# Kernel optimization log

Hardware: AMD Instinct MI355X
Metric: run time of the kernel (lower is better)

Reference implementation:

```python
import jax, jax.numpy as jnp
import numpy as np

SEQ, BATCH, IN_F, STATE, OUT_F = 2048, 32, 256, 512, 256


def setup_inputs() -> dict:
    key = jax.random.key(0)
    k1, k2, k3, k4 = jax.random.split(key, 4)
    x = jax.random.normal(k1, (SEQ, BATCH, IN_F), dtype=jnp.float32)
    # lambda_log init per module __init__ with rmin=0, rmax=1:
    # u ~ U(0,1); lambda_log = log(-0.5*log(u*(rmax+rmin)*(rmax-rmin)+rmin^2)) = log(-0.5*log(u))
    u = jax.random.uniform(k2, (STATE,), dtype=jnp.float32, minval=1e-6, maxval=1.0)
    lambda_log = jnp.log(-0.5 * jnp.log(u))
    B = jax.random.normal(k3, (STATE, IN_F), dtype=jnp.float32) / np.float32(np.sqrt(IN_F))
    C = jax.random.normal(k4, (OUT_F, STATE), dtype=jnp.float32) / np.float32(np.sqrt(STATE))
    return {"input": x, "lambda_log": lambda_log, "B": B, "C": C}


def reference(input, lambda_log, B, C):
    # mode='sequential', inner_loops=1, rnn_burnin=0, done=None, hidden=None
    lamda = jnp.exp(-jnp.exp(lambda_log))                 # [N]
    gamma = jnp.sqrt(1.0 - lamda * lamda + 1e-7)          # [N]
    # project all timesteps at once: b_seq[s,b,n] = gamma_n * (x_s @ B^T)
    b_seq = jnp.einsum('sbi,ni->sbn', input, B) * gamma   # [S,B,N]

    def step(state, b_t):
        new_state = lamda * state + b_t                   # diagonal LRU recurrence
        return new_state, new_state

    init = jnp.zeros((input.shape[1], lambda_log.shape[0]), dtype=input.dtype)
    final_state, states = jax.lax.scan(step, init, b_seq)  # states: [S,B,N]
    output = jnp.einsum('sbn,on->sbo', states, C)          # [S,B,O]
    return output, final_state
```

## Files before the change

kernel.cpp:

```cpp
#include <hip/hip_runtime.h>

#define SEQ   2048
#define BATCH 32
#define INF   256
#define NST   512
#define OUTF  256
#define CLEN  32
#define NCH   64
#define NJOB  4
#define NCG   (NCH / NJOB)
#define NBLK  (NCG * BATCH)

typedef __bf16 bf16;
typedef __bf16 bf16x8 __attribute__((ext_vector_type(8)));
typedef float  f32x4  __attribute__((ext_vector_type(4)));
typedef unsigned long long ull;

__global__ void k_prep(const float* __restrict__ ll,
                       const float* __restrict__ Bm,
                       const float* __restrict__ Cm,
                       float* __restrict__ lam,
                       float* __restrict__ lamG,
                       float* __restrict__ l2la,
                       bf16* __restrict__ Bb,
                       bf16* __restrict__ Cb) {
  int i = blockIdx.x * 256 + threadIdx.x;
  if (i < NST) {
    float e = expf(ll[i]);
    float lmb = expf(-e);
    lam[i] = lmb;
    l2la[i] = -e * 1.44269504088896341f;
    float p = lmb;
#pragma unroll
    for (int q = 0; q < 7; ++q) p *= p;
    lamG[i] = p;
  }
  if (i < NST * INF) {
    int n = i >> 8;
    float lmb = expf(-expf(ll[n]));
    float g = sqrtf(1.0f - lmb * lmb + 1e-7f);
    Bb[i] = (bf16)(Bm[i] * g);
  }
  if (i < OUTF * NST) {
    Cb[i] = (bf16)(Cm[i]);
  }
}

__device__ __forceinline__ void xload(const float* __restrict__ xp, int tid,
                                      float4 xr[4]) {
#pragma unroll
  for (int rep = 0; rep < 4; ++rep) {
    int slot = rep * 512 + tid;
    int row = slot >> 6, col4 = slot & 63;
    xr[rep] = *(const float4*)(xp + (size_t)row * (BATCH * INF) + col4 * 4);
  }
}

__device__ __forceinline__ void xstore(char* xsb, int tid, const float4 xr[4]) {
#pragma unroll
  for (int rep = 0; rep < 4; ++rep) {
    int slot = rep * 512 + tid;
    int row = slot >> 6, col4 = slot & 63;
    union { bf16 h[4]; ull u; } pk;
    pk.h[0] = (bf16)xr[rep].x; pk.h[1] = (bf16)xr[rep].y;
    pk.h[2] = (bf16)xr[rep].z; pk.h[3] = (bf16)xr[rep].w;
    int byte = (row * (INF * 2) + col4 * 8) ^ ((row & 15) << 4);
    *(ull*)(xsb + byte) = pk.u;
  }
}

__device__ __forceinline__ void reg_scan(f32x4 acc[2][4], float carry[4],
                                         const float la[4], const float l4[4],
                                         int kg, int rl) {
#pragma unroll
  for (int mt = 0; mt < 2; ++mt) {
    float sl[4][4];
#pragma unroll
    for (int nt = 0; nt < 4; ++nt) {
      sl[nt][0] = acc[mt][nt][0];
      sl[nt][1] = fmaf(la[nt], sl[nt][0], acc[mt][nt][1]);
      sl[nt][2] = fmaf(la[nt], sl[nt][1], acc[mt][nt][2]);
      sl[nt][3] = fmaf(la[nt], sl[nt][2], acc[mt][nt][3]);
    }
    float G[4];
#pragma unroll
    for (int nt = 0; nt < 4; ++nt) {
      float g1 = __shfl_up(sl[nt][3], 16);
      G[nt] = (kg >= 1) ? fmaf(l4[nt], g1, sl[nt][3]) : sl[nt][3];
    }
#pragma unroll
    for (int nt = 0; nt < 4; ++nt) {
      float l8 = l4[nt] * l4[nt];
      float g2 = __shfl_up(G[nt], 32);
      G[nt] = (kg >= 2) ? fmaf(l8, g2, G[nt]) : G[nt];
    }
#pragma unroll
    for (int nt = 0; nt < 4; ++nt) {
      float X = __shfl_up(G[nt], 16);
      X = (kg >= 1) ? X : 0.0f;
      float l8 = l4[nt] * l4[nt];
      float p4k = ((kg & 1) ? l4[nt] : 1.0f) * ((kg & 2) ? l8 : 1.0f);
      float cin = fmaf(p4k, carry[nt], X);
      float l2 = la[nt] * la[nt], l3 = l2 * la[nt];
      acc[mt][nt][0] = fmaf(la[nt], cin, sl[nt][0]);
      acc[mt][nt][1] = fmaf(l2, cin, sl[nt][1]);
      acc[mt][nt][2] = fmaf(l3, cin, sl[nt][2]);
      acc[mt][nt][3] = fmaf(l4[nt], cin, sl[nt][3]);
    }
#pragma unroll
    for (int nt = 0; nt < 4; ++nt)
      carry[nt] = __shfl(acc[mt][nt][3], rl + 48);
  }
}

__device__ __forceinline__ void gemm1_l2(const char* xsb, const bf16* __restrict__ Bb,
                                         f32x4 acc[2][4], int n0, int rl, int kg) {
#pragma unroll
  for (int k = 0; k < 8; ++k) {
    bf16x8 af[2], bfr[4];
#pragma unroll
    for (int mt = 0; mt < 2; ++mt) {
      int row = mt * 16 + rl;
      int byte = (row * (INF * 2) + (k * 32 + kg * 8) * 2) ^ (rl << 4);
      af[mt] = *(const bf16x8*)(xsb + byte);
    }
#pragma unroll
    for (int nt = 0; nt < 4; ++nt)
      bfr[nt] = *(const bf16x8*)(Bb + (size_t)(n0 + nt * 16 + rl) * INF + k * 32 + kg * 8);
#pragma unroll
    for (int mt = 0; mt < 2; ++mt)
#pragma unroll
      for (int nt = 0; nt < 4; ++nt)
        acc[mt][nt] = __builtin_amdgcn_mfma_f32_16x16x32_bf16(af[mt], bfr[nt], acc[mt][nt], 0, 0, 0);
  }
}

__global__ __launch_bounds__(512, 2)
void k_pass0f(const float* __restrict__ x, const bf16* __restrict__ Bb,
              const float* __restrict__ lam, float* __restrict__ Z,
              ull* __restrict__ bfrag) {
  __shared__ __align__(16) char xs[2][CLEN * INF * 2];

  const int tid = threadIdx.x, wid = tid >> 6, lane = tid & 63;
  const int rl = lane & 15, kg = lane >> 4;
  const int b = blockIdx.x >> 4, cg = blockIdx.x & 15;
  const int n0 = wid * 64;

  float la[4], l4[4], carry[4];
#pragma unroll
  for (int nt = 0; nt < 4; ++nt) {
    float v = lam[n0 + nt * 16 + rl];
    la[nt] = v; l4[nt] = (v * v) * (v * v);
    carry[nt] = 0.0f;
  }

  bf16x8 Breg[8][4];
#pragma unroll
  for (int k = 0; k < 8; ++k)
#pragma unroll
    for (int nt = 0; nt < 4; ++nt)
      Breg[k][nt] = *(const bf16x8*)(Bb + (size_t)(n0 + nt * 16 + rl) * INF + k * 32 + kg * 8);

  {
    float4 xr0[4];
    xload(x + ((size_t)(cg * NJOB * CLEN) * BATCH + b) * INF, tid, xr0);
    xstore(xs[0], tid, xr0);
  }
  __syncthreads();

#pragma unroll
  for (int jj = 0; jj < NJOB; ++jj) {
    const int c = cg * NJOB + jj;
    f32x4 acc[2][4] = {};
#pragma unroll
    for (int k = 0; k < 8; ++k) {
      bf16x8 af[2];
#pragma unroll
      for (int mt = 0; mt < 2; ++mt) {
        int row = mt * 16 + rl;
        int byte = (row * (INF * 2) + (k * 32 + kg * 8) * 2) ^ (rl << 4);
        af[mt] = *(const bf16x8*)(&xs[jj & 1][0] + byte);
      }
#pragma unroll
      for (int mt = 0; mt < 2; ++mt)
#pragma unroll
        for (int nt = 0; nt < 4; ++nt)
          acc[mt][nt] = __builtin_amdgcn_mfma_f32_16x16x32_bf16(af[mt], Breg[k][nt], acc[mt][nt], 0, 0, 0);
    }

    float4 xr[4];
    if (jj < NJOB - 1)
      xload(x + ((size_t)((c + 1) * CLEN) * BATCH + b) * INF, tid, xr);

    reg_scan(acc, carry, la, l4, kg, rl);

    {
      ull* dst = bfrag + ((size_t)(((cg * BATCH + b) * NJOB + jj) * 8 + wid)) * 512 + lane;
#pragma unroll
      for (int mt = 0; mt < 2; ++mt)
#pragma unroll
        for (int nt = 0; nt < 4; ++nt) {
          union { bf16 h[4]; ull u; } pk;
          pk.h[0] = (bf16)acc[mt][nt][0];
          pk.h[1] = (bf16)acc[mt][nt][1];
          pk.h[2] = (bf16)acc[mt][nt][2];
          pk.h[3] = (bf16)acc[mt][nt][3];
          dst[(mt * 4 + nt) * 64] = pk.u;
        }
    }

    if (jj < NJOB - 1) {
      xstore(xs[(jj + 1) & 1], tid, xr);
      __syncthreads();
    } else {
      if (kg == 0)
#pragma unroll
        for (int nt = 0; nt < 4; ++nt)
          Z[((size_t)cg * BATCH + b) * NST + n0 + nt * 16 + rl] = carry[nt];
    }
  }
}

__global__ __launch_bounds__(128)
void k_chain(const float* __restrict__ Z, const float* __restrict__ lamG,
             float* __restrict__ S0, float* __restrict__ fin) {
  const int b = blockIdx.x;
  const int n = blockIdx.y * 128 + threadIdx.x;
  const float lG = lamG[n];
  float z[NCG];
#pragma unroll
  for (int g = 0; g < NCG; ++g)
    z[g] = Z[((size_t)g * BATCH + b) * NST + n];
  float s = 0.0f;
#pragma unroll
  for (int g = 0; g < NCG; ++g) {
    S0[((size_t)g * BATCH + b) * NST + n] = s;
    s = fmaf(lG, s, z[g]);
  }
  fin[(size_t)b * NST + n] = s;
}

__global__ __launch_bounds__(512)
void k_gemm2c(const ull* __restrict__ bfrag, const bf16* __restrict__ Cb,
              const float* __restrict__ S0, const float* __restrict__ l2la,
              float* __restrict__ out) {
  __shared__ __align__(16) char ss[64 * NST * 2];

  const int tid = threadIdx.x, wid = tid >> 6, lane = tid & 63;
  const int rl = lane & 15, kg = lane >> 4;
  const int c2 = blockIdx.x >> 5, b = blockIdx.x & 31;
  const int cg = c2 >> 1;

  const ull* src8 = bfrag +
      ((size_t)((cg * BATCH + b) * NJOB + (c2 & 1) * 2)) * 4096;
  const float* S0g = S0 + ((size_t)cg * BATCH + b) * NST;
#pragma unroll
  for (int q = 0; q < 16; ++q) {
    int chunk = q * 512 + tid;
    int jjh = chunk >> 12;
    int within = chunk & 4095;
    int widx = within >> 9;
    int fr = (within >> 6) & 7;
    int mt = fr >> 2, nt = fr & 3;
    int ls = within & 63;
    int kgs = ls >> 4, rls = ls & 15;
    int n = widx * 64 + nt * 16 + rls;
    int t0 = jjh * 32 + mt * 16 + kgs * 4;
    int dt0 = (c2 & 1) * 64 + t0;

    union { ull u; bf16 h[4]; } in;
    in.u = src8[chunk];
    float l2 = l2la[n];
    float s0 = S0g[n];
    float e = exp2f((float)(dt0 + 1) * l2);
    float lm = exp2f(l2);
#pragma unroll
    for (int r = 0; r < 4; ++r) {
      float s = fmaf(e, s0, (float)in.h[r]);
      int t = t0 + r;
      int byte = (t * (NST * 2) + n * 2) ^ ((t & 15) << 4);
      *(bf16*)(&ss[0] + byte) = (bf16)s;
      e *= lm;
    }
  }
  __syncthreads();

  const int o0 = wid * 32;
  f32x4 acc[4][2] = {};
#pragma unroll
  for (int kq = 0; kq < 16; ++kq) {
    const int k0 = kq * 32;
    bf16x8 af[4], cf[2];
#pragma unroll
    for (int mf = 0; mf < 4; ++mf) {
      int t = mf * 16 + rl;
      af[mf] = *(const bf16x8*)(&ss[0] +
          ((t * (NST * 2) + (k0 + kg * 8) * 2) ^ ((t & 15) << 4)));
    }
#pragma unroll
    for (int ot2 = 0; ot2 < 2; ++ot2)
      cf[ot2] = *(const bf16x8*)(Cb + (size_t)(o0 + ot2 * 16 + rl) * NST + k0 + kg * 8);
#pragma unroll
    for (int mf = 0; mf < 4; ++mf)
#pragma unroll
      for (int ot2 = 0; ot2 < 2; ++ot2)
        acc[mf][ot2] = __builtin_amdgcn_mfma_f32_16x16x32_bf16(af[mf], cf[ot2], acc[mf][ot2], 0, 0, 0);
  }

#pragma unroll
  for (int mf = 0; mf < 4; ++mf)
#pragma unroll
    for (int ot2 = 0; ot2 < 2; ++ot2)
#pragma unroll
      for (int r = 0; r < 4; ++r) {
        int ml = mf * 16 + kg * 4 + r;
        size_t srow = (size_t)c2 * 64 + ml;
        int o = o0 + ot2 * 16 + rl;
        out[(srow * BATCH + b) * OUTF + o] = acc[mf][ot2][r];
      }
}

__global__ __launch_bounds__(512, 2)
void k_pass0_fb(const float* __restrict__ x, const bf16* __restrict__ Bb,
                const float* __restrict__ lam, float* __restrict__ Z) {
  __shared__ __align__(16) char xs[2][CLEN * INF * 2];

  const int tid = threadIdx.x, wid = tid >> 6, lane = tid & 63;
  const int rl = lane & 15, kg = lane >> 4;
  const int b = blockIdx.x >> 4, cg = blockIdx.x & 15;
  const int n0 = wid * 64;

  float la[4], l4[4], carry[4];
#pragma unroll
  for (int nt = 0; nt < 4; ++nt) {
    float v = lam[n0 + nt * 16 + rl];
    la[nt] = v; l4[nt] = (v * v) * (v * v);
    carry[nt] = 0.0f;
  }

  bf16x8 Breg[8][4];
#pragma unroll
  for (int k = 0; k < 8; ++k)
#pragma unroll
    for (int nt = 0; nt < 4; ++nt)
      Breg[k][nt] = *(const bf16x8*)(Bb + (size_t)(n0 + nt * 16 + rl) * INF + k * 32 + kg * 8);

  {
    float4 xr0[4];
    xload(x + ((size_t)(cg * NJOB * CLEN) * BATCH + b) * INF, tid, xr0);
    xstore(xs[0], tid, xr0);
  }
  __syncthreads();

#pragma unroll
  for (int jj = 0; jj < NJOB; ++jj) {
    const int c = cg * NJOB + jj;
    f32x4 acc[2][4] = {};
#pragma unroll
    for (int k = 0; k < 8; ++k) {
      bf16x8 af[2];
#pragma unroll
      for (int mt = 0; mt < 2; ++mt) {
        int row = mt * 16 + rl;
        int byte = (row * (INF * 2) + (k * 32 + kg * 8) * 2) ^ (rl << 4);
        af[mt] = *(const bf16x8*)(&xs[jj & 1][0] + byte);
      }
#pragma unroll
      for (int mt = 0; mt < 2; ++mt)
#pragma unroll
        for (int nt = 0; nt < 4; ++nt)
          acc[mt][nt] = __builtin_amdgcn_mfma_f32_16x16x32_bf16(af[mt], Breg[k][nt], acc[mt][nt], 0, 0, 0);
    }

    if (jj < NJOB - 1) {
      float4 xr[4];
      xload(x + ((size_t)((c + 1) * CLEN) * BATCH + b) * INF, tid, xr);
      reg_scan(acc, carry, la, l4, kg, rl);
      xstore(xs[(jj + 1) & 1], tid, xr);
      __syncthreads();
    } else {
      reg_scan(acc, carry, la, l4, kg, rl);
      if (kg == 0)
#pragma unroll
        for (int nt = 0; nt < 4; ++nt)
          Z[((size_t)cg * BATCH + b) * NST + n0 + nt * 16 + rl] = carry[nt];
    }
  }
}

__global__ __launch_bounds__(512)
void k_pass1_fb(const float* __restrict__ x, const bf16* __restrict__ Bb,
                const bf16* __restrict__ Cb, const float* __restrict__ lam,
                const float* __restrict__ S0, float* __restrict__ out,
                float* __restrict__ fin) {
  __shared__ __align__(16) char xs[2][CLEN * INF * 2];
  __shared__ __align__(16) char ss[CLEN * NST * 2];

  const int tid = threadIdx.x, wid = tid >> 6, lane = tid & 63;
  const int rl = lane & 15, kg = lane >> 4;
  const int b = blockIdx.x >> 4, cg = blockIdx.x & 15;
  const int n0 = wid * 64;

  float la[4], l4[4], carry[4];
#pragma unroll
  for (int nt = 0; nt < 4; ++nt) {
    float v = lam[n0 + nt * 16 + rl];
    la[nt] = v; l4[nt] = (v * v) * (v * v);
    carry[nt] = S0[((size_t)cg * BATCH + b) * NST + n0 + nt * 16 + rl];
  }
  {
    float4 xr0[4];
    xload(x + ((size_t)(cg * NJOB * CLEN) * BATCH + b) * INF, tid, xr0);
    xstore(xs[0], tid, xr0);
  }
  __syncthreads();

#pragma unroll
  for (int jj = 0; jj < NJOB; ++jj) {
    const int c = cg * NJOB + jj;
    f32x4 acc[2][4] = {};
    gemm1_l2(&xs[jj & 1][0], Bb, acc, n0, rl, kg);
    {
      float4 xr[4];
      const int lastj = (jj == NJOB - 1);
      if (!lastj)
        xload(x + ((size_t)((c + 1) * CLEN) * BATCH + b) * INF, tid, xr);
      reg_scan(acc, carry, la, l4, kg, rl);
      if (c == NCH - 1 && kg == 0)
#pragma unroll
        for (int nt = 0; nt < 4; ++nt)
          fin[(size_t)b * NST + n0 + nt * 16 + rl] = carry[nt];
      __syncthreads();
#pragma unroll
      for (int mt = 0; mt < 2; ++mt)
#pragma unroll
        for (int nt = 0; nt < 4; ++nt)
#pragma unroll
          for (int r = 0; r < 4; ++r) {
            int t = mt * 16 + kg * 4 + r;
            int n = n0 + nt * 16 + rl;
            int byte = (t * (NST * 2) + n * 2) ^ ((t & 15) << 4);
            *(bf16*)(&ss[0] + byte) = (bf16)acc[mt][nt][r];
          }
      if (!lastj) xstore(xs[(jj + 1) & 1], tid, xr);
    }
    __syncthreads();

    const int o0 = wid * 32;
    f32x4 a2[2][2] = {};
#pragma unroll
    for (int k0 = 0; k0 < NST; k0 += 32) {
      bf16x8 af[2], cf[2];
#pragma unroll
      for (int mt = 0; mt < 2; ++mt) {
        int t = mt * 16 + rl;
        int byte = (t * (NST * 2) + (k0 + kg * 8) * 2) ^ (rl << 4);
        af[mt] = *(const bf16x8*)(&ss[0] + byte);
      }
#pragma unroll
      for (int ot = 0; ot < 2; ++ot)
        cf[ot] = *(const bf16x8*)(Cb + (size_t)(o0 + ot * 16 + rl) * NST + k0 + kg * 8);
#pragma unroll
      for (int mt = 0; mt < 2; ++mt)
#pragma unroll
        for (int ot = 0; ot < 2; ++ot)
          a2[mt][ot] = __builtin_amdgcn_mfma_f32_16x16x32_bf16(af[mt], cf[ot], a2[mt][ot], 0, 0, 0);
    }
#pragma unroll
    for (int mt = 0; mt < 2; ++mt)
#pragma unroll
      for (int ot = 0; ot < 2; ++ot)
#pragma unroll
        for (int r = 0; r < 4; ++r) {
          int t = mt * 16 + kg * 4 + r;
          int o = o0 + ot * 16 + rl;
          out[(((size_t)(c * CLEN + t)) * BATCH + b) * OUTF + o] = a2[mt][ot][r];
        }
  }
}

extern "C" void kernel_launch(void* const* d_in, const int* in_sizes, int n_in,
                              void* d_out, int out_size, void* d_ws, size_t ws_size,
                              hipStream_t stream) {
  const float* x  = (const float*)d_in[0];
  const float* ll = (const float*)d_in[1];
  const float* Bm = (const float*)d_in[2];
  const float* Cm = (const float*)d_in[3];

  char* ws = (char*)d_ws;
  float* lam  = (float*)(ws);
  float* lamG = (float*)(ws + 2048);
  float* l2la = (float*)(ws + 4096);
  bf16*  Bb   = (bf16*)(ws + 6144);
  bf16*  Cb   = (bf16*)(ws + 6144 + NST * INF * 2);
  float* Z    = (float*)(ws + 6144 + NST * INF * 2 + OUTF * NST * 2);
  float* S0   = (float*)((char*)Z + (size_t)NCG * BATCH * NST * 4);
  ull*   bfrag= (ull*)((char*)S0 + (size_t)NCG * BATCH * NST * 4);
  const size_t NEED = ((char*)bfrag - ws) + (size_t)SEQ * BATCH * NST * 2;

  float* out = (float*)d_out;
  float* fin = out + (size_t)SEQ * BATCH * OUTF;

  k_prep<<<dim3(512), dim3(256), 0, stream>>>(ll, Bm, Cm, lam, lamG, l2la, Bb, Cb);
  if (ws_size >= NEED) {
    k_pass0f<<<dim3(NBLK), dim3(512), 0, stream>>>(x, Bb, lam, Z, bfrag);
    k_chain<<<dim3(BATCH, 4), dim3(128), 0, stream>>>(Z, lamG, S0, fin);
    k_gemm2c<<<dim3(1024), dim3(512), 0, stream>>>(bfrag, Cb, S0, l2la, out);
  } else {
    k_pass0_fb<<<dim3(NBLK), dim3(512), 0, stream>>>(x, Bb, lam, Z);
    k_chain<<<dim3(BATCH, 4), dim3(128), 0, stream>>>(Z, lamG, S0, fin);
    k_pass1_fb<<<dim3(NBLK), dim3(512), 0, stream>>>(x, Bb, Cb, lam, S0, out, fin);
  }
}
```

Before: 98.66 us.

## Precompute lambda power table, deepen x prefetch, software-pipeline C loads in GEMM2

k_prep now writes a per-state table of lambda^1..lambda^128, so the output GEMM reads decay factors instead of computing exp2 per element. In k_pass0f the x staging buffer grows from two to four LDS slots, so chunks are prefetched two ahead and the barrier moves earlier. The C-projection GEMM is hand-unrolled with a three-deep rotation of C fragment registers so global loads overlap the MFMAs. The trade-off is more LDS in pass0 (64KB, which may reduce occupancy at 2 blocks/CU), a serial 128-iteration loop per state in prep, and more register pressure.

Measured after the change: 110.4 us. 1.12x slower.

```diff
diff --git a/kernel.cpp b/kernel.cpp
--- a/kernel.cpp
+++ b/kernel.cpp
@@ -21,7 +21,7 @@
                        const float* __restrict__ Cm,
                        float* __restrict__ lam,
                        float* __restrict__ lamG,
-                       float* __restrict__ l2la,
+                       float* __restrict__ LamT,
                        bf16* __restrict__ Bb,
                        bf16* __restrict__ Cb) {
   int i = blockIdx.x * 256 + threadIdx.x;
@@ -29,11 +29,15 @@
     float e = expf(ll[i]);
     float lmb = expf(-e);
     lam[i] = lmb;
-    l2la[i] = -e * 1.44269504088896341f;
     float p = lmb;
 #pragma unroll
     for (int q = 0; q < 7; ++q) p *= p;
     lamG[i] = p;
+    float ee = lmb;
+    for (int dt = 0; dt < 128; ++dt) {
+      LamT[(size_t)i * 128 + dt] = ee;
+      ee *= lmb;
+    }
   }
   if (i < NST * INF) {
     int n = i >> 8;
@@ -139,7 +143,7 @@
 void k_pass0f(const float* __restrict__ x, const bf16* __restrict__ Bb,
               const float* __restrict__ lam, float* __restrict__ Z,
               ull* __restrict__ bfrag) {
-  __shared__ __align__(16) char xs[2][CLEN * INF * 2];
+  __shared__ __align__(16) char xs[4][CLEN * INF * 2];
 
   const int tid = threadIdx.x, wid = tid >> 6, lane = tid & 63;
   const int rl = lane & 15, kg = lane >> 4;
@@ -162,9 +166,11 @@
       Breg[k][nt] = *(const bf16x8*)(Bb + (size_t)(n0 + nt * 16 + rl) * INF + k * 32 + kg * 8);
 
   {
-    float4 xr0[4];
-    xload(x + ((size_t)(cg * NJOB * CLEN) * BATCH + b) * INF, tid, xr0);
-    xstore(xs[0], tid, xr0);
+    float4 xr[4];
+    xload(x + ((size_t)(cg * NJOB * CLEN) * BATCH + b) * INF, tid, xr);
+    xstore(xs[0], tid, xr);
+    xload(x + ((size_t)((cg * NJOB + 1) * CLEN) * BATCH + b) * INF, tid, xr);
+    xstore(xs[1], tid, xr);
   }
   __syncthreads();
 
@@ -179,7 +185,7 @@
       for (int mt = 0; mt < 2; ++mt) {
         int row = mt * 16 + rl;
         int byte = (row * (INF * 2) + (k * 32 + kg * 8) * 2) ^ (rl << 4);
-        af[mt] = *(const bf16x8*)(&xs[jj & 1][0] + byte);
+        af[mt] = *(const bf16x8*)(&xs[jj][0] + byte);
       }
 #pragma unroll
       for (int mt = 0; mt < 2; ++mt)
@@ -189,10 +195,15 @@
     }
 
     float4 xr[4];
-    if (jj < NJOB - 1)
-      xload(x + ((size_t)((c + 1) * CLEN) * BATCH + b) * INF, tid, xr);
+    if (jj < 2)
+      xload(x + ((size_t)((c + 2) * CLEN) * BATCH + b) * INF, tid, xr);
 
     reg_scan(acc, carry, la, l4, kg, rl);
+
+    if (jj < 2) {
+      xstore(xs[jj + 2], tid, xr);
+      __syncthreads();
+    }
 
     {
       ull* dst = bfrag + ((size_t)(((cg * BATCH + b) * NJOB + jj) * 8 + wid)) * 512 + lane;
@@ -209,10 +220,7 @@
         }
     }
 
-    if (jj < NJOB - 1) {
-      xstore(xs[(jj + 1) & 1], tid, xr);
-      __syncthreads();
-    } else {
+    if (jj == NJOB - 1) {
       if (kg == 0)
 #pragma unroll
         for (int nt = 0; nt < 4; ++nt)
@@ -241,8 +249,8 @@
 }
 
 __global__ __launch_bounds__(512)
-void k_gemm2c(const ull* __restrict__ bfrag, const bf16* __restrict__ Cb,
-              const float* __restrict__ S0, const float* __restrict__ l2la,
+void k_gemm2f(const ull* __restrict__ bfrag, const bf16* __restrict__ Cb,
+              const float* __restrict__ S0, const float* __restrict__ LamT,
               float* __restrict__ out) {
   __shared__ __align__(16) char ss[64 * NST * 2];
 
@@ -270,42 +278,60 @@
 
     union { ull u; bf16 h[4]; } in;
     in.u = src8[chunk];
-    float l2 = l2la[n];
+    float4 Lv = *(const float4*)(LamT + (size_t)n * 128 + dt0);
     float s0 = S0g[n];
-    float e = exp2f((float)(dt0 + 1) * l2);
-    float lm = exp2f(l2);
+    float lv[4] = {Lv.x, Lv.y, Lv.z, Lv.w};
 #pragma unroll
     for (int r = 0; r < 4; ++r) {
-      float s = fmaf(e, s0, (float)in.h[r]);
+      float s = fmaf(lv[r], s0, (float)in.h[r]);
       int t = t0 + r;
       int byte = (t * (NST * 2) + n * 2) ^ ((t & 15) << 4);
       *(bf16*)(&ss[0] + byte) = (bf16)s;
-      e *= lm;
     }
   }
   __syncthreads();
 
   const int o0 = wid * 32;
   f32x4 acc[4][2] = {};
-#pragma unroll
-  for (int kq = 0; kq < 16; ++kq) {
-    const int k0 = kq * 32;
-    bf16x8 af[4], cf[2];
-#pragma unroll
-    for (int mf = 0; mf < 4; ++mf) {
-      int t = mf * 16 + rl;
-      af[mf] = *(const bf16x8*)(&ss[0] +
-          ((t * (NST * 2) + (k0 + kg * 8) * 2) ^ ((t & 15) << 4)));
-    }
-#pragma unroll
-    for (int ot2 = 0; ot2 < 2; ++ot2)
-      cf[ot2] = *(const bf16x8*)(Cb + (size_t)(o0 + ot2 * 16 + rl) * NST + k0 + kg * 8);
-#pragma unroll
-    for (int mf = 0; mf < 4; ++mf)
-#pragma unroll
-      for (int ot2 = 0; ot2 < 2; ++ot2)
-        acc[mf][ot2] = __builtin_amdgcn_mfma_f32_16x16x32_bf16(af[mf], cf[ot2], acc[mf][ot2], 0, 0, 0);
-  }
+  bf16x8 cfp0[2], cfp1[2], cfp2[2];
+
+#define LOADC(CF, KQ) { \
+    CF[0] = *(const bf16x8*)(Cb + (size_t)(o0 + rl) * NST + (KQ) * 32 + kg * 8); \
+    CF[1] = *(const bf16x8*)(Cb + (size_t)(o0 + 16 + rl) * NST + (KQ) * 32 + kg * 8); }
+#define G2STEP(KQ, CF) { \
+    bf16x8 af0, af1, af2, af3; \
+    { int t = rl;      af0 = *(const bf16x8*)(&ss[0] + ((t * (NST*2) + ((KQ)*32 + kg*8)*2) ^ ((t & 15) << 4))); } \
+    { int t = 16 + rl; af1 = *(const bf16x8*)(&ss[0] + ((t * (NST*2) + ((KQ)*32 + kg*8)*2) ^ ((t & 15) << 4))); } \
+    { int t = 32 + rl; af2 = *(const bf16x8*)(&ss[0] + ((t * (NST*2) + ((KQ)*32 + kg*8)*2) ^ ((t & 15) << 4))); } \
+    { int t = 48 + rl; af3 = *(const bf16x8*)(&ss[0] + ((t * (NST*2) + ((KQ)*32 + kg*8)*2) ^ ((t & 15) << 4))); } \
+    acc[0][0] = __builtin_amdgcn_mfma_f32_16x16x32_bf16(af0, CF[0], acc[0][0], 0,0,0); \
+    acc[0][1] = __builtin_amdgcn_mfma_f32_16x16x32_bf16(af0, CF[1], acc[0][1], 0,0,0); \
+    acc[1][0] = __builtin_amdgcn_mfma_f32_16x16x32_bf16(af1, CF[0], acc[1][0], 0,0,0); \
+    acc[1][1] = __builtin_amdgcn_mfma_f32_16x16x32_bf16(af1, CF[1], acc[1][1], 0,0,0); \
+    acc[2][0] = __builtin_amdgcn_mfma_f32_16x16x32_bf16(af2, CF[0], acc[2][0], 0,0,0); \
+    acc[2][1] = __builtin_amdgcn_mfma_f32_16x16x32_bf16(af2, CF[1], acc[2][1], 0,0,0); \
+    acc[3][0] = __builtin_amdgcn_mfma_f32_16x16x32_bf16(af3, CF[0], acc[3][0], 0,0,0); \
+    acc[3][1] = __builtin_amdgcn_mfma_f32_16x16x32_bf16(af3, CF[1], acc[3][1], 0,0,0); }
+
+  LOADC(cfp0, 0) LOADC(cfp1, 1) LOADC(cfp2, 2)
+  G2STEP(0,  cfp0) LOADC(cfp0, 3)
+  G2STEP(1,  cfp1) LOADC(cfp1, 4)
+  G2STEP(2,  cfp2) LOADC(cfp2, 5)
+  G2STEP(3,  cfp0) LOADC(cfp0, 6)
+  G2STEP(4,  cfp1) LOADC(cfp1, 7)
+  G2STEP(5,  cfp2) LOADC(cfp2, 8)
+  G2STEP(6,  cfp0) LOADC(cfp0, 9)
+  G2STEP(7,  cfp1) LOADC(cfp1, 10)
+  G2STEP(8,  cfp2) LOADC(cfp2, 11)
+  G2STEP(9,  cfp0) LOADC(cfp0, 12)
+  G2STEP(10, cfp1) LOADC(cfp1, 13)
+  G2STEP(11, cfp2) LOADC(cfp2, 14)
+  G2STEP(12, cfp0) LOADC(cfp0, 15)
+  G2STEP(13, cfp1)
+  G2STEP(14, cfp2)
+  G2STEP(15, cfp0)
+#undef G2STEP
+#undef LOADC
 
 #pragma unroll
   for (int mf = 0; mf < 4; ++mf)
@@ -490,10 +516,10 @@
   char* ws = (char*)d_ws;
   float* lam  = (float*)(ws);
   float* lamG = (float*)(ws + 2048);
-  float* l2la = (float*)(ws + 4096);
-  bf16*  Bb   = (bf16*)(ws + 6144);
-  bf16*  Cb   = (bf16*)(ws + 6144 + NST * INF * 2);
-  float* Z    = (float*)(ws + 6144 + NST * INF * 2 + OUTF * NST * 2);
+  float* LamT = (float*)(ws + 4096);
+  bf16*  Bb   = (bf16*)(ws + 4096 + 262144);
+  bf16*  Cb   = (bf16*)((char*)Bb + (size_t)NST * INF * 2);
+  float* Z    = (float*)((char*)Cb + (size_t)OUTF * NST * 2);
   float* S0   = (float*)((char*)Z + (size_t)NCG * BATCH * NST * 4);
   ull*   bfrag= (ull*)((char*)S0 + (size_t)NCG * BATCH * NST * 4);
   const size_t NEED = ((char*)bfrag - ws) + (size_t)SEQ * BATCH * NST * 2;
@@ -501,11 +527,11 @@
   float* out = (float*)d_out;
   float* fin = out + (size_t)SEQ * BATCH * OUTF;
 
-  k_prep<<<dim3(512), dim3(256), 0, stream>>>(ll, Bm, Cm, lam, lamG, l2la, Bb, Cb);
+  k_prep<<<dim3(512), dim3(256), 0, stream>>>(ll, Bm, Cm, lam, lamG, LamT, Bb, Cb);
   if (ws_size >= NEED) {
     k_pass0f<<<dim3(NBLK), dim3(512), 0, stream>>>(x, Bb, lam, Z, bfrag);
     k_chain<<<dim3(BATCH, 4), dim3(128), 0, stream>>>(Z, lamG, S0, fin);
-    k_gemm2c<<<dim3(1024), dim3(512), 0, stream>>>(bfrag, Cb, S0, l2la, out);
+    k_gemm2f<<<dim3(1024), dim3(512), 0, stream>>>(bfrag, Cb, S0, LamT, out);
   } else {
     k_pass0_fb<<<dim3(NBLK), dim3(512), 0, stream>>>(x, Bb, lam, Z);
     k_chain<<<dim3(BATCH, 4), dim3(128), 0, stream>>>(Z, lamG, S0, fin);
```
